# Performance work log

Measured on AMD Instinct MI355X. Metric: run time of the kernel, lower is better.

## Reference

```python
import jax, jax.numpy as jnp
import numpy as np

EMBED = 256; HEADS = 8; LEVELS = 4; POINTS = 4; HID = 1024
HD = EMBED // HEADS
SHAPES = [(100, 100), (50, 50), (25, 25), (13, 13)]
STARTS = [0]
for _h, _w in SHAPES[:-1]:
    STARTS.append(STARTS[-1] + _h * _w)
TOTAL = sum(h * w for h, w in SHAPES)
BS = 2
EPS = 1e-5


def _ln(x, g, b):
    m = x.mean(-1, keepdims=True)
    v = ((x - m) ** 2).mean(-1, keepdims=True)
    return (x - m) / jnp.sqrt(v + EPS) * g + b


def _msda(query, value, ref, norm_wh, params):
    W_value, b_value, W_off, b_off, W_attn, b_attn, W_out, b_out = params
    bs, T, _ = query.shape
    v = (value @ W_value + b_value).reshape(bs, T, HEADS, HD)
    v = jnp.moveaxis(v, 2, 1)  # [bs, H, T, hd]
    off = (query @ W_off + b_off).reshape(bs, T, HEADS, LEVELS, POINTS, 2)
    aw = (query @ W_attn + b_attn).reshape(bs, T, HEADS, LEVELS * POINTS)
    aw = jax.nn.softmax(aw, axis=-1).reshape(bs, T, HEADS, LEVELS, POINTS)
    aw = jnp.moveaxis(aw, 2, 1)  # [bs, H, T, L, P]
    # sampling locations in [0,1] coords: ref + offset / (W_l, H_l)
    loc = ref[:, :, None, :, None, :] + off / norm_wh[None, None, None, :, None, :]
    loc = jnp.moveaxis(loc, 2, 1)  # [bs, H, T, L, P, 2]
    out = jnp.zeros((bs, HEADS, T, HD), query.dtype)
    for l, (Hl, Wl) in enumerate(SHAPES):
        s = STARTS[l]
        v_l = v[:, :, s:s + Hl * Wl]  # [bs, H, HW_l, hd]
        # grid_sample(align_corners=False): pixel = loc * size - 0.5
        x = loc[:, :, :, l, :, 0] * Wl - 0.5  # [bs, H, T, P]
        y = loc[:, :, :, l, :, 1] * Hl - 0.5
        x0 = jnp.floor(x); y0 = jnp.floor(y)
        wx1 = x - x0; wy1 = y - y0
        x0i = x0.astype(jnp.int32); y0i = y0.astype(jnp.int32)

        def samp(xi, yi):
            valid = (xi >= 0) & (xi < Wl) & (yi >= 0) & (yi < Hl)
            idx = jnp.clip(yi, 0, Hl - 1) * Wl + jnp.clip(xi, 0, Wl - 1)
            idx = idx.reshape(bs, HEADS, -1)
            g = jnp.take_along_axis(v_l, idx[..., None], axis=2)
            g = g.reshape(bs, HEADS, T, POINTS, HD)
            return g * valid[..., None].astype(g.dtype)

        bil = ((1 - wy1) * (1 - wx1))[..., None] * samp(x0i, y0i) \
            + ((1 - wy1) * wx1)[..., None] * samp(x0i + 1, y0i) \
            + (wy1 * (1 - wx1))[..., None] * samp(x0i, y0i + 1) \
            + (wy1 * wx1)[..., None] * samp(x0i + 1, y0i + 1)
        out = out + (bil * aw[:, :, :, l, :, None]).sum(axis=3)
    out = jnp.moveaxis(out, 1, 2).reshape(bs, T, EMBED)
    return out @ W_out + b_out


def setup_inputs() -> dict:
    key = jax.random.key(0)
    ks = jax.random.split(key, 16)
    s = 0.02
    f32 = jnp.float32
    return {
        "src": jax.random.normal(ks[0], (BS, TOTAL, EMBED), f32),
        "pos": jax.random.normal(ks[1], (BS, TOTAL, EMBED), f32),
        "reference_points": jax.random.uniform(ks[2], (BS, TOTAL, LEVELS, 2), f32),
        "spatial_shapes": jnp.array(SHAPES, jnp.int32),
        "level_start_index": jnp.array(STARTS, jnp.int32),
        "ln1_g": jnp.ones((EMBED,), f32), "ln1_b": jnp.zeros((EMBED,), f32),
        "ln2_g": jnp.ones((EMBED,), f32), "ln2_b": jnp.zeros((EMBED,), f32),
        "W_value": jax.random.normal(ks[3], (EMBED, EMBED), f32) * s,
        "b_value": jnp.zeros((EMBED,), f32),
        "W_off": jax.random.normal(ks[4], (EMBED, HEADS * LEVELS * POINTS * 2), f32) * s,
        "b_off": jax.random.normal(ks[5], (HEADS * LEVELS * POINTS * 2,), f32) * 0.5,
        "W_attn": jax.random.normal(ks[6], (EMBED, HEADS * LEVELS * POINTS), f32) * s,
        "b_attn": jnp.zeros((HEADS * LEVELS * POINTS,), f32),
        "W_out": jax.random.normal(ks[7], (EMBED, EMBED), f32) * s,
        "b_out": jnp.zeros((EMBED,), f32),
        "W_ffn1": jax.random.normal(ks[8], (EMBED, HID), f32) * s,
        "b_ffn1": jnp.zeros((HID,), f32),
        "W_ffn2": jax.random.normal(ks[9], (HID, EMBED), f32) * s,
        "b_ffn2": jnp.zeros((EMBED,), f32),
    }


def reference(src, pos, reference_points, spatial_shapes, level_start_index,
              ln1_g, ln1_b, ln2_g, ln2_b,
              W_value, b_value, W_off, b_off, W_attn, b_attn, W_out, b_out,
              W_ffn1, b_ffn1, W_ffn2, b_ffn2):
    src_n = _ln(src, ln1_g, ln1_b)
    q = src_n + pos
    # offset normalizer is (W_l, H_l)
    norm_wh = jnp.stack([spatial_shapes[:, 1], spatial_shapes[:, 0]], -1).astype(src.dtype)
    attn = _msda(q, src_n, reference_points, norm_wh,
                 (W_value, b_value, W_off, b_off, W_attn, b_attn, W_out, b_out))
    src1 = src + attn  # dropout = identity (eval)
    src_n2 = _ln(src1, ln2_g, ln2_b)
    ffn = jax.nn.relu(src_n2 @ W_ffn1 + b_ffn1) @ W_ffn2 + b_ffn2
    return src1 + ffn
```

## Files before the change

### kernel.cpp

```cpp
#include <hip/hip_runtime.h>
#include <hip/hip_bf16.h>

#define T_TOK   13294
#define BS_     2
#define M_ROWS  (BS_ * T_TOK)
#define EMBED_  256
#define HID_    1024

typedef __attribute__((ext_vector_type(8))) short short8;
typedef __attribute__((ext_vector_type(4))) float f32x4;

__device__ __forceinline__ unsigned short f2bf(float f) {
  __hip_bfloat16 h = __float2bfloat16(f);
  return *reinterpret_cast<unsigned short*>(&h);
}
__device__ __forceinline__ float bf2f(unsigned short u) {
  unsigned int x = ((unsigned int)u) << 16;
  return __uint_as_float(x);
}

__global__ __launch_bounds__(256) void transpose_all_kernel(
    const float* __restrict__ s0, const float* __restrict__ s1,
    const float* __restrict__ s2, const float* __restrict__ s3,
    const float* __restrict__ s4, const float* __restrict__ s5,
    unsigned short* __restrict__ d0, unsigned short* __restrict__ d1,
    unsigned short* __restrict__ d2, unsigned short* __restrict__ d3,
    unsigned short* __restrict__ d4, unsigned short* __restrict__ d5) {
  __shared__ float t[32][33];
  const int bid = blockIdx.x;
  const float* S; unsigned short* D; int K, N, t0;
  if      (bid <  64) { S = s0; D = d0; K = 256;  N = 256;  t0 = 0;   }
  else if (bid < 128) { S = s1; D = d1; K = 256;  N = 256;  t0 = 64;  }
  else if (bid < 160) { S = s2; D = d2; K = 256;  N = 128;  t0 = 128; }
  else if (bid < 224) { S = s3; D = d3; K = 256;  N = 256;  t0 = 160; }
  else if (bid < 480) { S = s4; D = d4; K = 256;  N = 1024; t0 = 224; }
  else                { S = s5; D = d5; K = 1024; N = 256;  t0 = 480; }
  const int tile = bid - t0;
  const int ntx = N >> 5;
  const int k0 = (tile / ntx) * 32, n0 = (tile % ntx) * 32;
  const int tx = threadIdx.x, ty = threadIdx.y;
  #pragma unroll
  for (int i = 0; i < 32; i += 8)
    t[ty + i][tx] = S[(size_t)(k0 + ty + i) * N + n0 + tx];
  __syncthreads();
  #pragma unroll
  for (int i = 0; i < 32; i += 8)
    D[(size_t)(n0 + ty + i) * K + k0 + tx] = f2bf(t[tx][ty + i]);
}

template <bool ADDPOS>
__global__ __launch_bounds__(256) void ln4_kernel(
    const float* __restrict__ x, const float* __restrict__ pos,
    const float* __restrict__ g, const float* __restrict__ bta,
    unsigned short* __restrict__ y, unsigned short* __restrict__ q) {
  const int wave = threadIdx.x >> 6, lane = threadIdx.x & 63;
  const int r = blockIdx.x * 4 + wave;
  const size_t base = (size_t)r * 256 + lane * 4;
  const float4 v = *reinterpret_cast<const float4*>(&x[base]);

  float s = v.x + v.y + v.z + v.w;
  #pragma unroll
  for (int m = 32; m; m >>= 1) s += __shfl_xor(s, m, 64);
  const float mean = s * (1.0f / 256.0f);

  const float dx = v.x - mean, dy = v.y - mean, dz = v.z - mean, dw = v.w - mean;
  float s2 = dx * dx + dy * dy + dz * dz + dw * dw;
  #pragma unroll
  for (int m = 32; m; m >>= 1) s2 += __shfl_xor(s2, m, 64);
  const float rinv = rsqrtf(s2 * (1.0f / 256.0f) + 1e-5f);

  const float4 gg = *reinterpret_cast<const float4*>(&g[lane * 4]);
  const float4 bb = *reinterpret_cast<const float4*>(&bta[lane * 4]);
  const float o0 = dx * rinv * gg.x + bb.x;
  const float o1 = dy * rinv * gg.y + bb.y;
  const float o2 = dz * rinv * gg.z + bb.z;
  const float o3 = dw * rinv * gg.w + bb.w;
  ushort4 yo; yo.x = f2bf(o0); yo.y = f2bf(o1); yo.z = f2bf(o2); yo.w = f2bf(o3);
  *reinterpret_cast<ushort4*>(&y[base]) = yo;
  if (ADDPOS) {
    const float4 pp = *reinterpret_cast<const float4*>(&pos[base]);
    ushort4 qo;
    qo.x = f2bf(o0 + pp.x); qo.y = f2bf(o1 + pp.y);
    qo.z = f2bf(o2 + pp.z); qo.w = f2bf(o3 + pp.w);
    *reinterpret_cast<ushort4*>(&q[base]) = qo;
  }
}

template <int EPI, bool OUTBF>
__device__ __forceinline__ void wgemm_core(
    const unsigned short* __restrict__ A, const unsigned short* __restrict__ Wt,
    const float* __restrict__ bias, const float* __restrict__ R,
    void* __restrict__ Cv, void* __restrict__ Cv2,
    int M, int N, int K, int row0, int col0, unsigned short* lds) {
  const int lane = threadIdx.x & 63;
  unsigned short* As = lds;
  unsigned short* Bs = lds + 64 * 32;

  f32x4 acc[4][4] = {};
  const int frow = lane & 15;
  const int fke = ((lane >> 4) ^ ((frow >> 1) & 3)) * 8;

  for (int k0 = 0; k0 < K; k0 += 32) {
    #pragma unroll
    for (int i = 0; i < 4; ++i) {
      const int chunk = i * 64 + lane;
      const int rrow = chunk >> 2;
      const int kgs = (chunk & 3) ^ ((rrow >> 1) & 3);
      int ga = row0 + rrow; if (ga >= M) ga = M - 1;
      __builtin_amdgcn_global_load_lds(
          (const __attribute__((address_space(1))) void*)(A + (size_t)ga * K + k0 + kgs * 8),
          (__attribute__((address_space(3))) void*)(As + chunk * 8), 16, 0, 0);
    }
    #pragma unroll
    for (int i = 0; i < 4; ++i) {
      const int chunk = i * 64 + lane;
      const int rrow = chunk >> 2;
      const int kgs = (chunk & 3) ^ ((rrow >> 1) & 3);
      __builtin_amdgcn_global_load_lds(
          (const __attribute__((address_space(1))) void*)(Wt + (size_t)(col0 + rrow) * K + k0 + kgs * 8),
          (__attribute__((address_space(3))) void*)(Bs + chunk * 8), 16, 0, 0);
    }
    asm volatile("s_waitcnt vmcnt(0)" ::: "memory");

    short8 a[4], b[4];
    #pragma unroll
    for (int mi = 0; mi < 4; ++mi)
      a[mi] = *reinterpret_cast<const short8*>(&As[(mi * 16 + frow) * 32 + fke]);
    #pragma unroll
    for (int ni = 0; ni < 4; ++ni)
      b[ni] = *reinterpret_cast<const short8*>(&Bs[(ni * 16 + frow) * 32 + fke]);
    #pragma unroll
    for (int mi = 0; mi < 4; ++mi)
      #pragma unroll
      for (int ni = 0; ni < 4; ++ni)
        acc[mi][ni] = __builtin_amdgcn_mfma_f32_16x16x32_bf16(b[ni], a[mi], acc[mi][ni], 0, 0, 0);
    asm volatile("s_waitcnt lgkmcnt(0)" ::: "memory");
  }

  const int lr = lane & 15;
  const int cb = (lane >> 4) * 4;
  #pragma unroll
  for (int mi = 0; mi < 4; ++mi) {
    const int grow = row0 + mi * 16 + lr;
    if (grow >= M) continue;
    #pragma unroll
    for (int ni = 0; ni < 4; ++ni) {
      const int gcol = col0 + ni * 16 + cb;
      float4 b4;
      if (EPI == 3) b4 = (gcol < 256) ? *reinterpret_cast<const float4*>(&bias[gcol])
                                      : *reinterpret_cast<const float4*>(&R[gcol - 256]);
      else          b4 = *reinterpret_cast<const float4*>(&bias[gcol]);
      float v0 = acc[mi][ni][0] + b4.x;
      float v1 = acc[mi][ni][1] + b4.y;
      float v2 = acc[mi][ni][2] + b4.z;
      float v3 = acc[mi][ni][3] + b4.w;
      if (EPI == 1) {
        v0 = fmaxf(v0, 0.f); v1 = fmaxf(v1, 0.f);
        v2 = fmaxf(v2, 0.f); v3 = fmaxf(v3, 0.f);
      }
      if (EPI == 2) {
        const float4 r4 = *reinterpret_cast<const float4*>(&R[(size_t)grow * N + gcol]);
        v0 += r4.x; v1 += r4.y; v2 += r4.z; v3 += r4.w;
        float4 o; o.x = v0; o.y = v1; o.z = v2; o.w = v3;
        *reinterpret_cast<float4*>(&((float*)Cv)[(size_t)grow * N + gcol]) = o;
      } else {
        ushort4 o;
        o.x = f2bf(v0); o.y = f2bf(v1); o.z = f2bf(v2); o.w = f2bf(v3);
        if (EPI == 3) {
          if (gcol < 256)
            *reinterpret_cast<ushort4*>(&((unsigned short*)Cv )[(size_t)grow * 256 + gcol]) = o;
          else
            *reinterpret_cast<ushort4*>(&((unsigned short*)Cv2)[(size_t)grow * 128 + gcol - 256]) = o;
        } else {
          *reinterpret_cast<ushort4*>(&((unsigned short*)Cv)[(size_t)grow * N + gcol]) = o;
        }
      }
    }
  }
}

template <int EPI, bool OUTBF>
__global__ __launch_bounds__(256) void wgemm_k(
    const unsigned short* __restrict__ A, const unsigned short* __restrict__ Wt,
    const float* __restrict__ bias, const float* __restrict__ R,
    void* __restrict__ Cv, int M, int N, int K) {
  __shared__ unsigned short lds[4 * 4096];
  const int w = threadIdx.x >> 6;
  const int nwg = gridDim.x;
  const int bid = blockIdx.x;
  const int wgid = (bid & 7) * (nwg >> 3) + (bid >> 3);
  const int tile = wgid * 4 + w;
  const int CT = N >> 6;
  const int row0 = (tile / CT) * 64;
  const int col0 = (tile % CT) * 64;
  wgemm_core<EPI, OUTBF>(A, Wt, bias, R, Cv, nullptr, M, N, K, row0, col0,
                         lds + w * 4096);
}

__global__ __launch_bounds__(256) void wproj_fused(
    const unsigned short* __restrict__ srcn, const unsigned short* __restrict__ q,
    const unsigned short* __restrict__ wt_val, const unsigned short* __restrict__ wt_offattn,
    const float* __restrict__ b_value, const float* __restrict__ b_off,
    const float* __restrict__ b_attn,
    unsigned short* __restrict__ vout, unsigned short* __restrict__ offout,
    unsigned short* __restrict__ awout, int M) {
  __shared__ unsigned short lds[4 * 4096];
  const int w = threadIdx.x >> 6;
  const int nwg = gridDim.x;
  const int bid = blockIdx.x;
  const int wgid = (bid & 7) * (nwg >> 3) + (bid >> 3);
  const int tile = wgid * 4 + w;
  if (tile < 1664) {
    const int row0 = (tile >> 2) * 64, col0 = (tile & 3) * 64;
    wgemm_core<0, true>(srcn, wt_val, b_value, nullptr, vout, nullptr,
                        M, 256, 256, row0, col0, lds + w * 4096);
  } else {
    const int t2 = tile - 1664;
    const int row0 = (t2 / 6) * 64, col0 = (t2 % 6) * 64;
    wgemm_core<3, false>(q, wt_offattn, b_off, b_attn, offout, awout,
                         M, 384, 256, row0, col0, lds + w * 4096);
  }
}

__global__ __launch_bounds__(256) void msda_kernel(
    const unsigned short* __restrict__ v, const unsigned short* __restrict__ offb,
    const unsigned short* __restrict__ awl, const float* __restrict__ ref,
    unsigned short* __restrict__ outb) {
  const int r0 = blockIdx.x * 8;
  const int tid = threadIdx.x;

  __shared__ float s_aw[8 * 128];
  __shared__ float s_ref[64];
  __shared__ float2 s_wi[64 * 66];

  if (tid < 64) {
    int rr = r0 + (tid >> 3); if (rr >= M_ROWS) rr = M_ROWS - 1;
    s_ref[tid] = ref[(size_t)rr * 8 + (tid & 7)];
  }

  {
    const int g = tid >> 2, j = tid & 3;
    const int tok = g >> 3, h = g & 7;
    int rr = r0 + tok; if (rr >= M_ROWS) rr = M_ROWS - 1;
    const uint2 u = *reinterpret_cast<const uint2*>(&awl[(size_t)rr * 128 + h * 16 + j * 4]);
    const float l0 = bf2f((unsigned short)(u.x & 0xffff));
    const float l1 = bf2f((unsigned short)(u.x >> 16));
    const float l2 = bf2f((unsigned short)(u.y & 0xffff));
    const float l3 = bf2f((unsigned short)(u.y >> 16));
    float mx = fmaxf(fmaxf(l0, l1), fmaxf(l2, l3));
    mx = fmaxf(mx, __shfl_xor(mx, 1, 64));
    mx = fmaxf(mx, __shfl_xor(mx, 2, 64));
    const float e0 = expf(l0 - mx), e1 = expf(l1 - mx);
    const float e2 = expf(l2 - mx), e3 = expf(l3 - mx);
    float ss = e0 + e1 + e2 + e3;
    ss += __shfl_xor(ss, 1, 64);
    ss += __shfl_xor(ss, 2, 64);
    const float inv = 1.0f / ss;
    float4 w4; w4.x = e0 * inv; w4.y = e1 * inv; w4.z = e2 * inv; w4.w = e3 * inv;
    *reinterpret_cast<float4*>(&s_aw[g * 16 + j * 4]) = w4;
  }
  __syncthreads();

  const int HH[4] = {100, 50, 25, 13};
  const int WW[4] = {100, 50, 25, 13};
  const int SS[4] = {0, 10000, 12500, 13125};

  {
    const int pi0 = tid * 4;
    const int tok = pi0 >> 7, h = (pi0 >> 4) & 7;
    const int g = pi0 >> 4;
    const int pt0 = pi0 & 15;
    const int l = pt0 >> 2;
    int rr = r0 + tok; if (rr >= M_ROWS) rr = M_ROWS - 1;
    const float Wl = (float)WW[l], Hl = (float)HH[l];
    const float rx = s_ref[tok * 8 + l * 2], ry = s_ref[tok * 8 + l * 2 + 1];
    const uint4 uoff = *reinterpret_cast<const uint4*>(&offb[(size_t)rr * 256 + h * 32 + pt0 * 2]);
    const float4 aw4 = *reinterpret_cast<const float4*>(&s_aw[g * 16 + pt0]);
    const unsigned int uo[4] = {uoff.x, uoff.y, uoff.z, uoff.w};
    const float awv[4] = {aw4.x, aw4.y, aw4.z, aw4.w};
    #pragma unroll
    for (int p = 0; p < 4; ++p) {
      const float ox = bf2f((unsigned short)(uo[p] & 0xffff));
      const float oy = bf2f((unsigned short)(uo[p] >> 16));
      const float x = rx * Wl + ox - 0.5f;
      const float y = ry * Hl + oy - 0.5f;
      const float x0f = floorf(x), y0f = floorf(y);
      const int x0 = (int)x0f, y0 = (int)y0f;
      const float wx1 = x - x0f, wy1 = y - y0f;
      const float wx0 = 1.f - wx1, wy0 = 1.f - wy1;
      const float aw = awv[p];
      #pragma unroll
      for (int c = 0; c < 4; ++c) {
        const int xx = x0 + (c & 1), yy = y0 + (c >> 1);
        const bool valid = (xx >= 0) & (xx < WW[l]) & (yy >= 0) & (yy < HH[l]);
        const int xc = min(max(xx, 0), WW[l] - 1);
        const int yc = min(max(yy, 0), HH[l] - 1);
        float wgt = aw * ((c & 1) ? wx1 : wx0) * ((c >> 1) ? wy1 : wy0);
        wgt = valid ? wgt : 0.f;
        const int idxb = (SS[l] + yc * WW[l] + xc) * 512;
        s_wi[g * 66 + (pt0 + p) * 4 + c] = make_float2(wgt, __int_as_float(idxb));
      }
    }
  }
  __syncthreads();

  const int tok = tid >> 5;
  const int h = (tid >> 2) & 7;
  const int d8 = tid & 3;
  const int r = r0 + tok;
  const int rc = (r < M_ROWS) ? r : M_ROWS - 1;
  const int b = rc / T_TOK;
  const char* vb = (const char*)(v + (size_t)b * T_TOK * 256 + h * 32 + d8 * 8);
  const int e0 = (tok * 8 + h) * 66;

  float a0 = 0.f, a1 = 0.f, a2 = 0.f, a3 = 0.f;
  float a4 = 0.f, a5 = 0.f, a6 = 0.f, a7 = 0.f;
  #pragma unroll 8
  for (int j = 0; j < 64; ++j) {
    const float2 wi = s_wi[e0 + j];
    const float wgt = wi.x;
    const int idxb = __float_as_int(wi.y);
    const uint4 u = *reinterpret_cast<const uint4*>(vb + idxb);
    a0 = fmaf(wgt, bf2f((unsigned short)(u.x & 0xffff)), a0);
    a1 = fmaf(wgt, bf2f((unsigned short)(u.x >> 16)), a1);
    a2 = fmaf(wgt, bf2f((unsigned short)(u.y & 0xffff)), a2);
    a3 = fmaf(wgt, bf2f((unsigned short)(u.y >> 16)), a3);
    a4 = fmaf(wgt, bf2f((unsigned short)(u.z & 0xffff)), a4);
    a5 = fmaf(wgt, bf2f((unsigned short)(u.z >> 16)), a5);
    a6 = fmaf(wgt, bf2f((unsigned short)(u.w & 0xffff)), a6);
    a7 = fmaf(wgt, bf2f((unsigned short)(u.w >> 16)), a7);
  }
  if (r < M_ROWS) {
    uint4 o;
    o.x = ((unsigned int)f2bf(a0)) | ((unsigned int)f2bf(a1) << 16);
    o.y = ((unsigned int)f2bf(a2)) | ((unsigned int)f2bf(a3) << 16);
    o.z = ((unsigned int)f2bf(a4)) | ((unsigned int)f2bf(a5) << 16);
    o.w = ((unsigned int)f2bf(a6)) | ((unsigned int)f2bf(a7) << 16);
    *reinterpret_cast<uint4*>(&outb[(size_t)r * 256 + h * 32 + d8 * 8]) = o;
  }
}

extern "C" void kernel_launch(void* const* d_in, const int* in_sizes, int n_in,
                              void* d_out, int out_size, void* d_ws, size_t ws_size,
                              hipStream_t stream) {
  const float* src     = (const float*)d_in[0];
  const float* pos     = (const float*)d_in[1];
  const float* ref     = (const float*)d_in[2];
  const float* ln1_g   = (const float*)d_in[5];
  const float* ln1_b   = (const float*)d_in[6];
  const float* ln2_g   = (const float*)d_in[7];
  const float* ln2_b   = (const float*)d_in[8];
  const float* W_value = (const float*)d_in[9];
  const float* b_value = (const float*)d_in[10];
  const float* W_off   = (const float*)d_in[11];
  const float* b_off   = (const float*)d_in[12];
  const float* W_attn  = (const float*)d_in[13];
  const float* b_attn  = (const float*)d_in[14];
  const float* W_out   = (const float*)d_in[15];
  const float* b_out   = (const float*)d_in[16];
  const float* W_ffn1  = (const float*)d_in[17];
  const float* b_ffn1  = (const float*)d_in[18];
  const float* W_ffn2  = (const float*)d_in[19];
  const float* b_ffn2  = (const float*)d_in[20];
  float* out = (float*)d_out;

  const int M = M_ROWS;
  const size_t n256 = (size_t)M * 256;

  unsigned short* src_n_bf = (unsigned short*)d_ws;
  unsigned short* q_bf     = src_n_bf + n256;
  unsigned short* v_bf     = q_bf + n256;
  unsigned short* attn_bf  = v_bf + n256;
  unsigned short* sn2_bf   = attn_bf + n256;
  unsigned short* hid_bf   = sn2_bf + n256;
  unsigned short* offb     = hid_bf + (size_t)M * 1024;
  unsigned short* awbuf    = offb + n256;
  float* src1 = (float*)(awbuf + (size_t)M * 128);
  unsigned short* wt_val     = (unsigned short*)(src1 + n256);
  unsigned short* wt_offattn = wt_val + 256 * 256;
  unsigned short* wt_out     = wt_offattn + 384 * 256;
  unsigned short* wt_ffn1    = wt_out + 256 * 256;
  unsigned short* wt_ffn2    = wt_ffn1 + 1024 * 256;

  transpose_all_kernel<<<736, dim3(32, 8), 0, stream>>>(
      W_value, W_off, W_attn, W_out, W_ffn1, W_ffn2,
      wt_val, wt_offattn, wt_offattn + 256 * 256, wt_out, wt_ffn1, wt_ffn2);

  ln4_kernel<true><<<M / 4, 256, 0, stream>>>(src, pos, ln1_g, ln1_b, src_n_bf, q_bf);

  wproj_fused<<<1040, 256, 0, stream>>>(
      src_n_bf, q_bf, wt_val, wt_offattn, b_value, b_off, b_attn,
      v_bf, offb, awbuf, M);

  msda_kernel<<<(M + 7) / 8, 256, 0, stream>>>(v_bf, offb, awbuf, ref, attn_bf);

  wgemm_k<2, false><<<416, 256, 0, stream>>>(attn_bf, wt_out, b_out, src,
                                             src1, M, 256, 256);

  ln4_kernel<false><<<M / 4, 256, 0, stream>>>(src1, nullptr, ln2_g, ln2_b, sn2_bf, nullptr);

  wgemm_k<1, true ><<<1664, 256, 0, stream>>>(sn2_bf, wt_ffn1, b_ffn1, nullptr,
                                              hid_bf, M, 1024, 256);
  wgemm_k<2, false><<<416, 256, 0, stream>>>(hid_bf, wt_ffn2, b_ffn2, src1,
                                             out, M, 256, 1024);
}
```

Measured before the change: 201.9 us.

## Fuse output projection with LayerNorm and overlap GEMM loads with MFMA

Adds an outln_kernel that computes the attention output projection, adds bias and residual, writes src1, and computes LayerNorm2 in the epilogue. Row statistics are reduced across the four waves through shared memory, which removes a separate LN kernel launch and its reread of src1. Separately, the GEMM core now issues the next K-slice's global-to-LDS loads after the fragment reads and before the MFMAs, so loads overlap compute. That prefetch writes into the same single LDS buffer, so correctness relies on the fragment reads completing first. LN variance is now computed as E[x^2]-mean^2 in one pass, which is less numerically stable than the old two-pass form.

```diff
diff --git a/kernel.cpp b/kernel.cpp
--- a/kernel.cpp
+++ b/kernel.cpp
@@ -86,6 +86,31 @@
   }
 }
 
+__device__ __forceinline__ void stage64(
+    const unsigned short* __restrict__ A, const unsigned short* __restrict__ Wt,
+    unsigned short* As, unsigned short* Bs,
+    int M, int K, int row0, int col0, int k0, int lane) {
+  #pragma unroll
+  for (int i = 0; i < 4; ++i) {
+    const int chunk = i * 64 + lane;
+    const int rrow = chunk >> 2;
+    const int kgs = (chunk & 3) ^ ((rrow >> 1) & 3);
+    int ga = row0 + rrow; if (ga >= M) ga = M - 1;
+    __builtin_amdgcn_global_load_lds(
+        (const __attribute__((address_space(1))) void*)(A + (size_t)ga * K + k0 + kgs * 8),
+        (__attribute__((address_space(3))) void*)(As + chunk * 8), 16, 0, 0);
+  }
+  #pragma unroll
+  for (int i = 0; i < 4; ++i) {
+    const int chunk = i * 64 + lane;
+    const int rrow = chunk >> 2;
+    const int kgs = (chunk & 3) ^ ((rrow >> 1) & 3);
+    __builtin_amdgcn_global_load_lds(
+        (const __attribute__((address_space(1))) void*)(Wt + (size_t)(col0 + rrow) * K + k0 + kgs * 8),
+        (__attribute__((address_space(3))) void*)(Bs + chunk * 8), 16, 0, 0);
+  }
+}
+
 template <int EPI, bool OUTBF>
 __device__ __forceinline__ void wgemm_core(
     const unsigned short* __restrict__ A, const unsigned short* __restrict__ Wt,
@@ -100,28 +125,10 @@
   const int frow = lane & 15;
   const int fke = ((lane >> 4) ^ ((frow >> 1) & 3)) * 8;
 
+  stage64(A, Wt, As, Bs, M, K, row0, col0, 0, lane);
+  asm volatile("s_waitcnt vmcnt(0)" ::: "memory");
+
   for (int k0 = 0; k0 < K; k0 += 32) {
-    #pragma unroll
-    for (int i = 0; i < 4; ++i) {
-      const int chunk = i * 64 + lane;
-      const int rrow = chunk >> 2;
-      const int kgs = (chunk & 3) ^ ((rrow >> 1) & 3);
-      int ga = row0 + rrow; if (ga >= M) ga = M - 1;
-      __builtin_amdgcn_global_load_lds(
-          (const __attribute__((address_space(1))) void*)(A + (size_t)ga * K + k0 + kgs * 8),
-          (__attribute__((address_space(3))) void*)(As + chunk * 8), 16, 0, 0);
-    }
-    #pragma unroll
-    for (int i = 0; i < 4; ++i) {
-      const int chunk = i * 64 + lane;
-      const int rrow = chunk >> 2;
-      const int kgs = (chunk & 3) ^ ((rrow >> 1) & 3);
-      __builtin_amdgcn_global_load_lds(
-          (const __attribute__((address_space(1))) void*)(Wt + (size_t)(col0 + rrow) * K + k0 + kgs * 8),
-          (__attribute__((address_space(3))) void*)(Bs + chunk * 8), 16, 0, 0);
-    }
-    asm volatile("s_waitcnt vmcnt(0)" ::: "memory");
-
     short8 a[4], b[4];
     #pragma unroll
     for (int mi = 0; mi < 4; ++mi)
@@ -129,12 +136,20 @@
     #pragma unroll
     for (int ni = 0; ni < 4; ++ni)
       b[ni] = *reinterpret_cast<const short8*>(&Bs[(ni * 16 + frow) * 32 + fke]);
+    asm volatile("s_waitcnt lgkmcnt(0)" ::: "memory");
+    __builtin_amdgcn_sched_barrier(0);
+
+    if (k0 + 32 < K)
+      stage64(A, Wt, As, Bs, M, K, row0, col0, k0 + 32, lane);
+
     #pragma unroll
     for (int mi = 0; mi < 4; ++mi)
       #pragma unroll
       for (int ni = 0; ni < 4; ++ni)
         acc[mi][ni] = __builtin_amdgcn_mfma_f32_16x16x32_bf16(b[ni], a[mi], acc[mi][ni], 0, 0, 0);
-    asm volatile("s_waitcnt lgkmcnt(0)" ::: "memory");
+
+    if (k0 + 32 < K)
+      asm volatile("s_waitcnt vmcnt(0)" ::: "memory");
   }
 
   const int lr = lane & 15;
@@ -222,6 +237,119 @@
   }
 }
 
+__global__ __launch_bounds__(256) void outln_kernel(
+    const unsigned short* __restrict__ attn, const unsigned short* __restrict__ wt_out,
+    const float* __restrict__ b_out, const float* __restrict__ src,
+    const float* __restrict__ ln_g, const float* __restrict__ ln_b,
+    float* __restrict__ src1, unsigned short* __restrict__ sn2, int M) {
+  __shared__ unsigned short lds[4 * 4096];
+  __shared__ float s_sum[64][4];
+  __shared__ float s_sq[64][4];
+  const int w = threadIdx.x >> 6, lane = threadIdx.x & 63;
+  const int nwg = gridDim.x;
+  const int bid = blockIdx.x;
+  const int wgid = (bid & 7) * (nwg >> 3) + (bid >> 3);
+  const int row0 = wgid * 64;
+  const int col0 = w * 64;
+  unsigned short* As = lds + w * 4096;
+  unsigned short* Bs = As + 64 * 32;
+
+  f32x4 acc[4][4] = {};
+  const int frow = lane & 15;
+  const int fke = ((lane >> 4) ^ ((frow >> 1) & 3)) * 8;
+
+  stage64(attn, wt_out, As, Bs, M, 256, row0, col0, 0, lane);
+  asm volatile("s_waitcnt vmcnt(0)" ::: "memory");
+  for (int k0 = 0; k0 < 256; k0 += 32) {
+    short8 a[4], b[4];
+    #pragma unroll
+    for (int mi = 0; mi < 4; ++mi)
+      a[mi] = *reinterpret_cast<const short8*>(&As[(mi * 16 + frow) * 32 + fke]);
+    #pragma unroll
+    for (int ni = 0; ni < 4; ++ni)
+      b[ni] = *reinterpret_cast<const short8*>(&Bs[(ni * 16 + frow) * 32 + fke]);
+    asm volatile("s_waitcnt lgkmcnt(0)" ::: "memory");
+    __builtin_amdgcn_sched_barrier(0);
+    if (k0 + 32 < 256)
+      stage64(attn, wt_out, As, Bs, M, 256, row0, col0, k0 + 32, lane);
+    #pragma unroll
+    for (int mi = 0; mi < 4; ++mi)
+      #pragma unroll
+      for (int ni = 0; ni < 4; ++ni)
+        acc[mi][ni] = __builtin_amdgcn_mfma_f32_16x16x32_bf16(b[ni], a[mi], acc[mi][ni], 0, 0, 0);
+    if (k0 + 32 < 256)
+      asm volatile("s_waitcnt vmcnt(0)" ::: "memory");
+  }
+
+  const int lr = lane & 15;
+  const int cb = (lane >> 4) * 4;
+  float lsum[4], lsq[4];
+  #pragma unroll
+  for (int mi = 0; mi < 4; ++mi) {
+    const int grow = row0 + mi * 16 + lr;
+    const bool ok = grow < M;
+    float rs = 0.f, rq = 0.f;
+    #pragma unroll
+    for (int ni = 0; ni < 4; ++ni) {
+      const int gcol = col0 + ni * 16 + cb;
+      const float4 b4 = *reinterpret_cast<const float4*>(&b_out[gcol]);
+      float4 r4 = make_float4(0.f, 0.f, 0.f, 0.f);
+      if (ok) r4 = *reinterpret_cast<const float4*>(&src[(size_t)grow * 256 + gcol]);
+      float v0 = acc[mi][ni][0] + b4.x + r4.x;
+      float v1 = acc[mi][ni][1] + b4.y + r4.y;
+      float v2 = acc[mi][ni][2] + b4.z + r4.z;
+      float v3 = acc[mi][ni][3] + b4.w + r4.w;
+      acc[mi][ni][0] = v0; acc[mi][ni][1] = v1;
+      acc[mi][ni][2] = v2; acc[mi][ni][3] = v3;
+      if (ok) {
+        float4 o; o.x = v0; o.y = v1; o.z = v2; o.w = v3;
+        *reinterpret_cast<float4*>(&src1[(size_t)grow * 256 + gcol]) = o;
+      }
+      rs += v0 + v1 + v2 + v3;
+      rq += v0 * v0 + v1 * v1 + v2 * v2 + v3 * v3;
+    }
+    lsum[mi] = rs; lsq[mi] = rq;
+  }
+  #pragma unroll
+  for (int mi = 0; mi < 4; ++mi) {
+    lsum[mi] += __shfl_xor(lsum[mi], 16, 64);
+    lsum[mi] += __shfl_xor(lsum[mi], 32, 64);
+    lsq[mi]  += __shfl_xor(lsq[mi], 16, 64);
+    lsq[mi]  += __shfl_xor(lsq[mi], 32, 64);
+  }
+  if (lane < 16) {
+    #pragma unroll
+    for (int mi = 0; mi < 4; ++mi) {
+      s_sum[mi * 16 + lane][w] = lsum[mi];
+      s_sq[mi * 16 + lane][w] = lsq[mi];
+    }
+  }
+  __syncthreads();
+  #pragma unroll
+  for (int mi = 0; mi < 4; ++mi) {
+    const int lrow = mi * 16 + lr;
+    const int grow = row0 + lrow;
+    if (grow >= M) continue;
+    const float s = s_sum[lrow][0] + s_sum[lrow][1] + s_sum[lrow][2] + s_sum[lrow][3];
+    const float q = s_sq[lrow][0] + s_sq[lrow][1] + s_sq[lrow][2] + s_sq[lrow][3];
+    const float mean = s * (1.0f / 256.0f);
+    const float var = q * (1.0f / 256.0f) - mean * mean;
+    const float rinv = rsqrtf(var + 1e-5f);
+    #pragma unroll
+    for (int ni = 0; ni < 4; ++ni) {
+      const int gcol = col0 + ni * 16 + cb;
+      const float4 g4 = *reinterpret_cast<const float4*>(&ln_g[gcol]);
+      const float4 bb = *reinterpret_cast<const float4*>(&ln_b[gcol]);
+      ushort4 o;
+      o.x = f2bf((acc[mi][ni][0] - mean) * rinv * g4.x + bb.x);
+      o.y = f2bf((acc[mi][ni][1] - mean) * rinv * g4.y + bb.y);
+      o.z = f2bf((acc[mi][ni][2] - mean) * rinv * g4.z + bb.z);
+      o.w = f2bf((acc[mi][ni][3] - mean) * rinv * g4.w + bb.w);
+      *reinterpret_cast<ushort4*>(&sn2[(size_t)grow * 256 + gcol]) = o;
+    }
+  }
+}
+
 __global__ __launch_bounds__(256) void msda_kernel(
     const unsigned short* __restrict__ v, const unsigned short* __restrict__ offb,
     const unsigned short* __restrict__ awl, const float* __restrict__ ref,
@@ -394,10 +522,8 @@
 
   msda_kernel<<<(M + 7) / 8, 256, 0, stream>>>(v_bf, offb, awbuf, ref, attn_bf);
 
-  wgemm_k<2, false><<<416, 256, 0, stream>>>(attn_bf, wt_out, b_out, src,
-                                             src1, M, 256, 256);
-
-  ln4_kernel<false><<<M / 4, 256, 0, stream>>>(src1, nullptr, ln2_g, ln2_b, sn2_bf, nullptr);
+  outln_kernel<<<416, 256, 0, stream>>>(attn_bf, wt_out, b_out, src,
+                                        ln2_g, ln2_b, src1, sn2_bf, M);
 
   wgemm_k<1, true ><<<1664, 256, 0, stream>>>(sn2_bf, wt_ffn1, b_ffn1, nullptr,
                                               hid_bf, M, 1024, 256);
```

New measurement: 200.1 us. Within noise of the previous version (-0.9%).
